# Optimization experiments

Measured on AMD Instinct MI355X. Metric: run time of the kernel, lower is better.

Reference implementation:

```python
import jax, jax.numpy as jnp
import numpy as np
import math
from functools import lru_cache

# ---- static configuration (matches init_kwargs) ----
B_IN = 24           # input bandwidth  -> spatial grid 2*B_IN = 48
B_OUT = 24          # output bandwidth (<= B_IN)
F_IN = 16           # nfeature_in
F_OUT = 16          # output_dim
BATCH = 16
N_ALPHA = 6
_alphas = np.arange(N_ALPHA) * (2.0 * np.pi / N_ALPHA)
_betas_g = np.array([np.pi / 16.0, np.pi / 8.0])
GRID = np.array([[a, b, 0.0] for a in _alphas for b in _betas_g])  # [12, 3] = (alpha, beta, gamma)
SCALING = 1.0 / math.sqrt(GRID.shape[0] * F_IN * (B_OUT ** 3) / (B_IN ** 3))

_LNF = np.array([math.lgamma(n + 1.0) for n in range(4 * max(B_IN, B_OUT) + 4)])  # log n!


def _wigner_d(l, beta):
    """Wigner small-d matrix d^l_{m'm}(beta); element [l+m', l+m]. numpy, float64."""
    m = np.arange(-l, l + 1)
    mp = m[:, None, None]          # m'
    mm = m[None, :, None]          # m
    k = np.arange(0, 2 * l + 1)[None, None, :]
    valid = (k >= np.maximum(0, mm - mp)) & (k <= np.minimum(l + mm, l - mp))
    kk = np.where(valid, k, 0)
    ln = (0.5 * (_LNF[l + mp] + _LNF[l - mp] + _LNF[l + mm] + _LNF[l - mm])
          - _LNF[np.where(valid, l + mm - k, 0)] - _LNF[kk]
          - _LNF[np.where(valid, mp - mm + k, 0)] - _LNF[np.where(valid, l - mp - k, 0)])
    sign = np.where((mp - mm + k) % 2 == 0, 1.0, -1.0)
    coef = np.where(valid, sign * np.exp(ln), 0.0)
    c, s = np.cos(beta / 2.0), np.sin(beta / 2.0)
    e_c = np.where(valid, 2 * l - 2 * k + mm - mp, 0)
    e_s = np.where(valid, 2 * k + mp - mm, 0)
    return (coef * (c ** e_c) * (s ** e_s)).sum(-1)  # [2l+1, 2l+1]


def _quad_weights(b):
    """Driscoll-Healy quadrature weights over beta, scaled so that
    sum_j w_j d^l_{mn}(b_j) d^{l'}_{mn}(b_j) = delta_{ll'} / (2l+1)."""
    k = np.arange(b)
    j = np.arange(2 * b)
    s = np.sin(np.outer(2 * j + 1, 2 * k + 1) * np.pi / (4.0 * b))
    w = (2.0 / b) * np.sin(np.pi * (2 * j + 1) / (4.0 * b)) * (s / (2 * k + 1)).sum(1)
    return w / 2.0


@lru_cache(maxsize=None)
def _wigner_betas(b, nl, weighted):
    """Per-degree wigner-d stacks at SOFT beta grid: tuple of [2b, 2l+1, 2l+1]."""
    betas = (np.arange(2 * b) + 0.5) * np.pi / (2 * b)
    w = _quad_weights(b)
    out = []
    for l in range(nl):
        d = np.stack([_wigner_d(l, be) for be in betas])  # [2b, 2l+1, 2l+1]
        d = d * (w[:, None, None] if weighted else float(2 * l + 1))
        out.append(jnp.asarray(d.astype(np.float32)))
    return tuple(out)


@lru_cache(maxsize=None)
def _so3_rft_matrix(b):
    """conj(D^l_{mn}(g_p)) for each grid rotation; [P, nspec] complex64."""
    mats = []
    for l in range(b):
        m = np.arange(-l, l + 1)
        rows = []
        for (al, be, ga) in GRID:
            D = np.exp(-1j * m[:, None] * al) * _wigner_d(l, be) * np.exp(-1j * m[None, :] * ga)
            rows.append(np.conj(D).reshape(-1))
        mats.append(np.stack(rows))  # [P, (2l+1)^2]
    return jnp.asarray(np.concatenate(mats, axis=1).astype(np.complex64))


def so3_rfft(x, b_out):
    # x: [Z, 2b, 2b, 2b] real, axes = (beta, alpha, gamma) -> [nspec, Z] complex
    b_in = x.shape[1] // 2
    X = jnp.fft.fftn(x.astype(jnp.complex64), axes=(2, 3))  # [Z, beta, m, n]
    wig = _wigner_betas(b_in, b_out, True)
    outs = []
    for l in range(b_out):
        idx = np.arange(-l, l + 1) % (2 * b_in)             # static FFT freq indices
        xx = X[:, :, idx[:, None], idx[None, :]]            # [Z, 2b, 2l+1, 2l+1]
        Fl = jnp.einsum('jmn,zjmn->mnz', wig[l], xx)        # beta quadrature
        outs.append(Fl.reshape((2 * l + 1) ** 2, -1))
    return jnp.concatenate(outs, axis=0)


def so3_mm(Fx, Fy, b):
    # Fx [nspec, B, f_in], Fy [nspec, f_in, f_out] -> [nspec, B, f_out]; per-degree block matmul
    outs, begin = [], 0
    for l in range(b):
        L = 2 * l + 1
        xl = Fx[begin:begin + L * L].reshape(L, L, Fx.shape[1], Fx.shape[2])
        yl = Fy[begin:begin + L * L].reshape(L, L, Fy.shape[1], Fy.shape[2])
        zl = jnp.einsum('mkbf,knfg->mnbg', xl, yl)
        outs.append(zl.reshape(L * L, Fx.shape[1], Fy.shape[2]))
        begin += L * L
    return jnp.concatenate(outs, axis=0)


def so3_rifft(Fz, b):
    # Fz [nspec, Z] complex -> [Z, 2b, 2b, 2b] real
    Z = Fz.shape[1]
    wig = _wigner_betas(b, b, False)
    S = jnp.zeros((Z, 2 * b, 2 * b, 2 * b), jnp.complex64)
    begin = 0
    for l in range(b):
        L = 2 * l + 1
        Fl = Fz[begin:begin + L * L].reshape(L, L, Z)
        sl = jnp.einsum('jmn,mnz->zjmn', wig[l], Fl)
        idx = np.arange(-l, l + 1) % (2 * b)
        S = S.at[:, :, idx[:, None], idx[None, :]].add(sl)
        begin += L * L
    return jnp.fft.ifftn(S, axes=(2, 3)).real.astype(jnp.float32)


def _forward(x, kernel):
    B = x.shape[0]
    z = x.reshape(B * F_IN, 2 * B_IN, 2 * B_IN, 2 * B_IN)
    Fx = so3_rfft(z, B_OUT).reshape(-1, B, F_IN)                      # [nspec, B, f_in]
    Fy = jnp.einsum('fgp,ps->sfg', (kernel * SCALING).astype(jnp.complex64),
                    _so3_rft_matrix(B_OUT))                           # [nspec, f_in, f_out]
    Fz = so3_mm(Fx, Fy, B_OUT)                                        # [nspec, B, f_out]
    out = so3_rifft(Fz.reshape(-1, B * F_OUT), B_OUT)
    return out.reshape(B, F_OUT, 2 * B_OUT, 2 * B_OUT, 2 * B_OUT)


def setup_inputs() -> dict:
    key = jax.random.key(0)
    k1, k2 = jax.random.split(key)
    x = jax.random.normal(k1, (BATCH, F_IN, 2 * B_IN, 2 * B_IN, 2 * B_IN), jnp.float32)
    kernel = jax.random.normal(k2, (F_IN, F_OUT, GRID.shape[0]), jnp.float32) * 0.05
    return {"x": x, "kernel": kernel}


def reference(x, kernel):
    return _forward(x, kernel)
```

## Files before the change

### kernel.cpp

```cpp
#include <hip/hip_runtime.h>
#include <math.h>

#define NSPEC 18424

static constexpr int OFF[25] = {0,1,10,35,84,165,286,455,680,969,1330,1771,2300,2925,
                                3654,4495,5456,6545,7770,9139,10660,12341,14190,16215,18424};
static constexpr int BACC[25] = {0,1,2,6,10,19,28,44,60,85,110,146,182,231,280,344,
                                 408,489,570,670,770,891,1012,1156,1300};
static constexpr double PI_D = 3.14159265358979323846264338327950288;
static constexpr float SCALING_F = 0.07216878364870322f;

__device__ __forceinline__ void cfma(float2& acc, float2 a, float2 b){
    acc.x += a.x*b.x - a.y*b.y;
    acc.y += a.x*b.y + a.y*b.x;
}

__global__ __launch_bounds__(256) void k0_wigner(float* __restrict__ wig_w,
                                                 float* __restrict__ wig_u,
                                                 float2* __restrict__ conjD){
    const int l = blockIdx.x, bi = blockIdx.y, L = 2*l+1;
    __shared__ double lnf[104];
    const int t = threadIdx.x;
    for (int i = t; i < 104; i += 256){
        double s = 0.0;
        for (int k = 2; k <= i; ++k) s += log((double)k);
        lnf[i] = s;
    }
    __syncthreads();
    double beta, alpha = 0.0, wq = 0.0;
    const bool isq = (bi < 48);
    if (isq){
        beta = (bi + 0.5)*PI_D/48.0;
        double acc = 0.0;
        for (int k = 0; k < 24; ++k)
            acc += sin((double)(2*bi+1)*(double)(2*k+1)*PI_D/96.0)/(double)(2*k+1);
        wq = (2.0/24.0)*sin(PI_D*(double)(2*bi+1)/96.0)*acc*0.5;
    } else {
        int p = bi - 48;
        alpha = (double)(p >> 1)*(PI_D/3.0);
        beta  = (p & 1) ? PI_D/8.0 : PI_D/16.0;
    }
    const double ch = cos(0.5*beta), sh = sin(0.5*beta);
    const double lc = log(ch), ls = log(sh);
    for (int e = t; e < L*L; e += 256){
        const int r = e / L, c = e % L;
        const int mp = r - l, mm = c - l;
        const int k0 = max(0, mm - mp), k1 = min(l + mm, l - mp);
        const double pre = 0.5*(lnf[l+mp] + lnf[l-mp] + lnf[l+mm] + lnf[l-mm]);
        double d = 0.0;
        for (int k = k0; k <= k1; ++k){
            const int ec = 2*l - 2*k + mm - mp, es = 2*k + mp - mm;
            const double term = exp(pre - lnf[l+mm-k] - lnf[k] - lnf[mp-mm+k]
                                    - lnf[l-mp-k] + (double)ec*lc + (double)es*ls);
            d += ((mp - mm + k) & 1) ? -term : term;
        }
        if (isq){
            const int idx = 48*OFF[l] + (bi*L + r)*L + c;
            wig_w[idx] = (float)(wq*d);
            wig_u[idx] = (float)((double)(2*l+1)*d);
        } else {
            const int p = bi - 48;
            conjD[(size_t)p*NSPEC + OFF[l] + r*L + c] =
                make_float2((float)(cos((double)mp*alpha)*d),
                            (float)(sin((double)mp*alpha)*d));
        }
    }
}

__global__ __launch_bounds__(256) void k_twiddles(float2* __restrict__ tw1a,
                                                  float2* __restrict__ tw1b,
                                                  float2* __restrict__ twI1,
                                                  float2* __restrict__ twI2){
    const int t = threadIdx.x;
    for (int i = t; i < 24*48; i += 256){
        int m = i/48, a = i%48;
        double th = 2.0*PI_D*(double)(m*a)/48.0;
        tw1a[i] = make_float2((float)cos(th), (float)(-sin(th)));
        twI2[i] = make_float2((float)cos(th), (float)sin(th));
    }
    for (int i = t; i < 48*48; i += 256){
        int n = i/48, c = i%48;
        double th = 2.0*PI_D*(double)(n*c)/48.0;
        tw1b[i] = make_float2((float)cos(th), (float)(-sin(th)));
    }
    for (int i = t; i < 47*48; i += 256){
        int nn = i/48, c = i%48;
        double th = 2.0*PI_D*(double)((nn-23)*c)/48.0;
        twI1[i] = make_float2((float)cos(th), (float)sin(th));
    }
}

__global__ __launch_bounds__(192) void k1a(const float* __restrict__ x,
                                           const float2* __restrict__ tw1a,
                                           float2* __restrict__ A1){
    const int j = blockIdx.x, z = blockIdx.y;
    __shared__ float xs[48*49];
    __shared__ float2 tws[24*48];
    for (int e = threadIdx.x; e < 1152; e += 192) tws[e] = tw1a[e];
    const float* src = x + (size_t)(z*48 + j)*2304;
    for (int e = threadIdx.x; e < 2304; e += 192)
        xs[(e/48)*49 + (e%48)] = src[e];
    __syncthreads();
    const int c = threadIdx.x % 48, mq = threadIdx.x / 48;
    float ar[6], ai[6];
    #pragma unroll
    for (int i = 0; i < 6; ++i){ ar[i] = 0.f; ai[i] = 0.f; }
    for (int a = 0; a < 48; ++a){
        const float xv = xs[a*49 + c];
        #pragma unroll
        for (int i = 0; i < 6; ++i){
            const float2 tw = tws[(mq*6 + i)*48 + a];
            ar[i] += xv*tw.x; ai[i] += xv*tw.y;
        }
    }
    #pragma unroll
    for (int i = 0; i < 6; ++i){
        const int m = mq*6 + i;
        A1[((size_t)(j*24 + m)*256 + z)*48 + c] = make_float2(ar[i], ai[i]);
    }
}

__global__ __launch_bounds__(256) void k1b(const float2* __restrict__ A1,
                                           const float2* __restrict__ tw1b,
                                           float2* __restrict__ Xf){
    const int m = blockIdx.x, j = blockIdx.y, zt = blockIdx.z;
    __shared__ float2 as_[48*129];
    __shared__ float2 tws[48*48];
    for (int e = threadIdx.x; e < 2304; e += 256) tws[e] = tw1b[e];
    const float2* src = A1 + ((size_t)(j*24 + m)*256 + zt*128)*48;
    for (int e = threadIdx.x; e < 6144; e += 256)
        as_[(e%48)*129 + (e/48)] = src[e];
    __syncthreads();
    const int z = threadIdx.x & 127, nh = threadIdx.x >> 7;
    float2 acc[24];
    #pragma unroll
    for (int i = 0; i < 24; ++i) acc[i] = make_float2(0.f, 0.f);
    for (int cc = 0; cc < 48; ++cc){
        const float2 xv = as_[cc*129 + z];
        #pragma unroll
        for (int i = 0; i < 24; ++i)
            cfma(acc[i], xv, tws[(nh*24 + i)*48 + cc]);
    }
    #pragma unroll
    for (int i = 0; i < 24; ++i){
        const int n = nh*24 + i;
        Xf[((size_t)(j*24 + m)*48 + n)*256 + zt*128 + z] = acc[i];
    }
}

__global__ __launch_bounds__(256) void k2(const float2* __restrict__ Xf,
                                          const float* __restrict__ wigw,
                                          float2* __restrict__ Fx){
    const int mf = (int)blockIdx.x - 23, nf = (int)blockIdx.y - 23;
    const int z = threadIdx.x;
    const int am = mf < 0 ? -mf : mf;
    const int anf = nf < 0 ? -nf : nf;
    const int lmin = am > anf ? am : anf;
    const int nidx = ((mf < 0 ? -nf : nf) + 48) % 48;
    const float sgn = mf < 0 ? -1.f : 1.f;
    float ar[24], ai[24];
    int widx[24];
    #pragma unroll
    for (int l = 0; l < 24; ++l){
        ar[l] = 0.f; ai[l] = 0.f;
        widx[l] = 48*OFF[l] + (l+mf)*(2*l+1) + (l+nf);
    }
    for (int j = 0; j < 48; ++j){
        const float2 xv = Xf[((size_t)(j*24 + am)*48 + nidx)*256 + z];
        const float xi = sgn*xv.y;
        #pragma unroll
        for (int l = 0; l < 24; ++l){
            if (l >= lmin){
                const float w = wigw[widx[l]];
                ar[l] += w*xv.x; ai[l] += w*xi;
            }
            widx[l] += (2*l+1)*(2*l+1);
        }
    }
    #pragma unroll
    for (int l = 0; l < 24; ++l){
        if (l >= lmin){
            const int L = 2*l+1;
            Fx[((size_t)(OFF[l] + (l+mf)*L + (l+nf)))*256 + z] = make_float2(ar[l], ai[l]);
        }
    }
}

__global__ __launch_bounds__(256) void k3(const float* __restrict__ kern,
                                          const float2* __restrict__ conjD,
                                          float2* __restrict__ Fy){
    const int s = blockIdx.x, t = threadIdx.x;
    float kr[12];
    #pragma unroll
    for (int p = 0; p < 12; ++p) kr[p] = kern[t*12 + p];
    float accr = 0.f, acci = 0.f;
    #pragma unroll
    for (int p = 0; p < 12; ++p){
        const float2 D = conjD[(size_t)p*NSPEC + s];
        accr += kr[p]*D.x; acci += kr[p]*D.y;
    }
    Fy[(size_t)s*256 + t] = make_float2(SCALING_F*accr, SCALING_F*acci);
}

__global__ __launch_bounds__(256) void k4g(const float2* __restrict__ Fx,
                                           const float2* __restrict__ Fy,
                                           float2* __restrict__ Fz){
    const int bid = blockIdx.x;
    int l = 0;
    #pragma unroll
    for (int i = 1; i < 24; ++i) if (bid >= BACC[i]) l = i;
    const int L = 2*l+1, CT = l/2 + 1;
    const int tb = bid - BACC[l];
    const int bm = tb / CT, bn = tb % CT;
    const int t = threadIdx.x;
    const int lane = t & 63, seg = t >> 6;
    const int tr = t >> 4, tc = t & 15;
    __shared__ float2 As[16*64];
    __shared__ float2 Bs[16*64];
    float2 acc[4][4];
    #pragma unroll
    for (int i = 0; i < 4; ++i)
        #pragma unroll
        for (int jj = 0; jj < 4; ++jj) acc[i][jj] = make_float2(0.f, 0.f);

    const int mr = bm*4 + seg;
    const int nc = bn*4 + seg;
    const bool va = (mr < L), vb = (nc < L);
    const float2* aPtr = Fx + (size_t)(OFF[l] + (va ? mr : 0)*L)*256 + lane*4;
    const float2* bPtr = Fy + (size_t)(OFF[l] + (vb ? nc : 0))*256 + lane*4;
    const int bA  = lane >> 2;
    const int fA0 = (lane & 3)*4;
    const int fB  = lane >> 2;
    const int gB0 = (lane & 3)*4;

    for (int k = 0; k < L; ++k){
        float2 a0={0,0},a1={0,0},a2={0,0},a3={0,0};
        float2 b0={0,0},b1={0,0},b2={0,0},b3={0,0};
        if (va){ const float2* p = aPtr + (size_t)k*256; a0=p[0]; a1=p[1]; a2=p[2]; a3=p[3]; }
        if (vb){ const float2* p = bPtr + (size_t)k*L*256; b0=p[0]; b1=p[1]; b2=p[2]; b3=p[3]; }
        __syncthreads();
        As[(fA0+0)*64 + seg*16 + bA] = a0;
        As[(fA0+1)*64 + seg*16 + bA] = a1;
        As[(fA0+2)*64 + seg*16 + bA] = a2;
        As[(fA0+3)*64 + seg*16 + bA] = a3;
        Bs[fB*64 + seg*16 + gB0 + 0] = b0;
        Bs[fB*64 + seg*16 + gB0 + 1] = b1;
        Bs[fB*64 + seg*16 + gB0 + 2] = b2;
        Bs[fB*64 + seg*16 + gB0 + 3] = b3;
        __syncthreads();
        #pragma unroll
        for (int f = 0; f < 16; ++f){
            float2 av0 = As[f*64 + tr*4 + 0];
            float2 av1 = As[f*64 + tr*4 + 1];
            float2 av2 = As[f*64 + tr*4 + 2];
            float2 av3 = As[f*64 + tr*4 + 3];
            float2 bv0 = Bs[f*64 + tc*4 + 0];
            float2 bv1 = Bs[f*64 + tc*4 + 1];
            float2 bv2 = Bs[f*64 + tc*4 + 2];
            float2 bv3 = Bs[f*64 + tc*4 + 3];
            cfma(acc[0][0], av0, bv0); cfma(acc[0][1], av0, bv1);
            cfma(acc[0][2], av0, bv2); cfma(acc[0][3], av0, bv3);
            cfma(acc[1][0], av1, bv0); cfma(acc[1][1], av1, bv1);
            cfma(acc[1][2], av1, bv2); cfma(acc[1][3], av1, bv3);
            cfma(acc[2][0], av2, bv0); cfma(acc[2][1], av2, bv1);
            cfma(acc[2][2], av2, bv2); cfma(acc[2][3], av2, bv3);
            cfma(acc[3][0], av3, bv0); cfma(acc[3][1], av3, bv1);
            cfma(acc[3][2], av3, bv2); cfma(acc[3][3], av3, bv3);
        }
    }
    #pragma unroll
    for (int i = 0; i < 4; ++i){
        const int r = tr*4 + i;
        const int mro = bm*4 + (r >> 4), b = r & 15;
        if (mro < L){
            #pragma unroll
            for (int jj = 0; jj < 4; ++jj){
                const int c = tc*4 + jj;
                const int nco = bn*4 + (c >> 4), g = c & 15;
                if (nco < L)
                    Fz[((size_t)(OFF[l] + mro*L + nco))*256 + b*16 + g] = acc[i][jj];
            }
        }
    }
}

__global__ __launch_bounds__(256) void k5(const float2* __restrict__ Fz,
                                          const float* __restrict__ wigu,
                                          float2* __restrict__ S){
    const int mf = blockIdx.x;
    const int nf = (int)blockIdx.y - 23;
    const int z = threadIdx.x;
    const int anf = nf < 0 ? -nf : nf;
    const int lmin = mf > anf ? mf : anf;
    float2 fz[24];
    int widx[24];
    #pragma unroll
    for (int l = 0; l < 24; ++l){
        const int L = 2*l+1;
        fz[l] = (l >= lmin) ? Fz[((size_t)(OFF[l] + (l+mf)*L + (l+nf)))*256 + z]
                            : make_float2(0.f, 0.f);
        widx[l] = 48*OFF[l] + (l+mf)*L + (l+nf);
    }
    const int nn = nf + 23;
    for (int j = 0; j < 48; ++j){
        float sr = 0.f, si = 0.f;
        #pragma unroll
        for (int l = 0; l < 24; ++l){
            if (l >= lmin){
                const float w = wigu[widx[l]];
                sr += w*fz[l].x; si += w*fz[l].y;
            }
            widx[l] += (2*l+1)*(2*l+1);
        }
        S[((size_t)(mf*47 + nn)*48 + j)*256 + z] = make_float2(sr, si);
    }
}

__global__ __launch_bounds__(256) void i1(const float2* __restrict__ S,
                                          const float2* __restrict__ twI1,
                                          float2* __restrict__ U){
    const int m = blockIdx.x, j = blockIdx.y, zt = blockIdx.z;
    __shared__ float2 sbuf[128*49];
    __shared__ float2 tws[47*48];
    for (int e = threadIdx.x; e < 2256; e += 256) tws[e] = twI1[e];
    for (int e = threadIdx.x; e < 47*128; e += 256){
        const int nn = e >> 7, zl = e & 127;
        sbuf[nn*128 + zl] = S[((size_t)(m*47 + nn)*48 + j)*256 + zt*128 + zl];
    }
    __syncthreads();
    const int z = threadIdx.x & 127, ch = threadIdx.x >> 7;
    float2 acc[24];
    #pragma unroll
    for (int i = 0; i < 24; ++i) acc[i] = make_float2(0.f, 0.f);
    for (int nn = 0; nn < 47; ++nn){
        const float2 sv = sbuf[nn*128 + z];
        #pragma unroll
        for (int i = 0; i < 24; ++i)
            cfma(acc[i], sv, tws[nn*48 + ch*24 + i]);
    }
    __syncthreads();
    #pragma unroll
    for (int i = 0; i < 24; ++i)
        sbuf[z*49 + ch*24 + i] = acc[i];
    __syncthreads();
    float2* dst = U + (size_t)(j*256 + zt*128)*1152 + m*48;
    for (int e = threadIdx.x; e < 6144; e += 256){
        const int zz = e/48, c = e%48;
        dst[(size_t)zz*1152 + c] = sbuf[zz*49 + c];
    }
}

__global__ __launch_bounds__(256) void i2(const float2* __restrict__ U,
                                          const float2* __restrict__ twI2,
                                          float* __restrict__ out){
    const int z = blockIdx.x, j = blockIdx.y;
    __shared__ float2 uv[24*49];
    __shared__ float2 tws[24*48];
    for (int e = threadIdx.x; e < 1152; e += 256) tws[e] = twI2[e];
    const float2* src = U + (size_t)(j*256 + z)*1152;
    for (int e = threadIdx.x; e < 1152; e += 256)
        uv[(e/48)*49 + (e%48)] = src[e];
    __syncthreads();
    float* dst = out + (size_t)(z*48 + j)*2304;
    for (int o = threadIdx.x; o < 2304; o += 256){
        const int a = o / 48, c = o % 48;
        float acc = uv[c].x;
        #pragma unroll
        for (int m = 1; m < 24; ++m){
            const float2 tw = tws[m*48 + a];
            const float2 u  = uv[m*49 + c];
            acc += 2.0f*(tw.x*u.x - tw.y*u.y);
        }
        dst[o] = acc*(1.0f/2304.0f);
    }
}

extern "C" void kernel_launch(void* const* d_in, const int* in_sizes, int n_in,
                              void* d_out, int out_size, void* d_ws, size_t ws_size,
                              hipStream_t stream){
    (void)in_sizes; (void)n_in; (void)out_size;
    const float* x    = (const float*)d_in[0];
    const float* kern = (const float*)d_in[1];
    float* out = (float*)d_out;

    char* ws = (char*)d_ws;
    size_t o = 0;
    auto nb = [&](size_t bytes){ size_t r = o; o += (bytes + 255) & ~(size_t)255; return r; };
    float*  wig_w = (float*) (ws + nb(884352ull*4));
    float*  wig_u = (float*) (ws + nb(884352ull*4));
    float2* conjD = (float2*)(ws + nb(221088ull*8));
    float2* tw1a  = (float2*)(ws + nb(1152ull*8));
    float2* tw1b  = (float2*)(ws + nb(2304ull*8));
    float2* twI1  = (float2*)(ws + nb(2256ull*8));
    float2* twI2  = (float2*)(ws + nb(1152ull*8));
    float2* big0  = (float2*)(ws + nb(14155776ull*8));
    float2* big1  = (float2*)(ws + nb(14155776ull*8));
    float2* Fx    = (float2*)(ws + nb(4716544ull*8));
    float2* Fy    = (float2*)(ws + nb(4716544ull*8));
    float2* Fz    = (float2*)(ws + nb(4716544ull*8));
    if (o > ws_size) return;

    k0_wigner <<<dim3(24,60),  dim3(256), 0, stream>>>(wig_w, wig_u, conjD);
    k_twiddles<<<dim3(1),      dim3(256), 0, stream>>>(tw1a, tw1b, twI1, twI2);
    k1a       <<<dim3(48,256), dim3(192), 0, stream>>>(x, tw1a, big0);
    k1b       <<<dim3(24,48,2),dim3(256), 0, stream>>>(big0, tw1b, big1);
    k2        <<<dim3(47,47),  dim3(256), 0, stream>>>(big1, wig_w, Fx);
    k3        <<<dim3(NSPEC),  dim3(256), 0, stream>>>(kern, conjD, Fy);
    k4g       <<<dim3(1300),   dim3(256), 0, stream>>>(Fx, Fy, Fz);
    k5        <<<dim3(24,47),  dim3(256), 0, stream>>>(Fz, wig_u, big0);
    i1        <<<dim3(24,48,2),dim3(256), 0, stream>>>(big0, twI1, big1);
    i2        <<<dim3(256,48), dim3(256), 0, stream>>>(big1, twI2, out);
}
```

Before: 1.823 ms.

## Exploit conjugate symmetry in k2/k4g, recurrence Wigner-d, drop twiddle LDS copies

```diff
diff --git a/kernel.cpp b/kernel.cpp
--- a/kernel.cpp
+++ b/kernel.cpp
@@ -5,8 +5,8 @@
 
 static constexpr int OFF[25] = {0,1,10,35,84,165,286,455,680,969,1330,1771,2300,2925,
                                 3654,4495,5456,6545,7770,9139,10660,12341,14190,16215,18424};
-static constexpr int BACC[25] = {0,1,2,6,10,19,28,44,60,85,110,146,182,231,280,344,
-                                 408,489,570,670,770,891,1012,1156,1300};
+static constexpr int P24[25] = {0,72,144,210,276,326,376,421,466,498,530,558,586,604,622,
+                                637,652,660,668,674,680,682,684,685,686};
 static constexpr double PI_D = 3.14159265358979323846264338327950288;
 static constexpr float SCALING_F = 0.07216878364870322f;
 
@@ -15,17 +15,47 @@
     acc.y += a.x*b.y + a.y*b.x;
 }
 
-__global__ __launch_bounds__(256) void k0_wigner(float* __restrict__ wig_w,
+__global__ __launch_bounds__(256) void k_tables(float2* __restrict__ tw1a,
+                                                float2* __restrict__ tw1b,
+                                                float2* __restrict__ twI1,
+                                                float2* __restrict__ twI2,
+                                                double* __restrict__ lnfg){
+    const int t = threadIdx.x;
+    __shared__ double lt[104];
+    if (t < 104) lt[t] = (t >= 2) ? log((double)t) : 0.0;
+    __syncthreads();
+    if (t == 0){
+        double run = 0.0;
+        for (int i = 0; i < 104; ++i){ run += lt[i]; lnfg[i] = run; }
+    }
+    for (int i = t; i < 24*48; i += 256){
+        int m = i/48, a = i%48;
+        double th = 2.0*PI_D*(double)(m*a)/48.0;
+        tw1a[i] = make_float2((float)cos(th), (float)(-sin(th)));
+        twI2[i] = make_float2((float)cos(th), (float)sin(th));
+    }
+    for (int i = t; i < 48*48; i += 256){
+        int n = i/48, c = i%48;
+        double th = 2.0*PI_D*(double)(n*c)/48.0;
+        tw1b[i] = make_float2((float)cos(th), (float)(-sin(th)));
+    }
+    for (int i = t; i < 47*48; i += 256){
+        int nn = i/48, c = i%48;
+        double th = 2.0*PI_D*(double)((nn-23)*c)/48.0;
+        twI1[i] = make_float2((float)cos(th), (float)sin(th));
+    }
+}
+
+__global__ __launch_bounds__(256) void k0_wigner(const double* __restrict__ lnfg,
+                                                 float* __restrict__ wig_w,
                                                  float* __restrict__ wig_u,
                                                  float2* __restrict__ conjD){
     const int l = blockIdx.x, bi = blockIdx.y, L = 2*l+1;
     __shared__ double lnf[104];
+    __shared__ double rcpt[105];
     const int t = threadIdx.x;
-    for (int i = t; i < 104; i += 256){
-        double s = 0.0;
-        for (int k = 2; k <= i; ++k) s += log((double)k);
-        lnf[i] = s;
-    }
+    for (int i = t; i < 104; i += 256) lnf[i] = lnfg[i];
+    for (int i = t; i < 105; i += 256) rcpt[i] = (i > 0) ? 1.0/(double)i : 0.0;
     __syncthreads();
     double beta, alpha = 0.0, wq = 0.0;
     const bool isq = (bi < 48);
@@ -42,17 +72,27 @@
     }
     const double ch = cos(0.5*beta), sh = sin(0.5*beta);
     const double lc = log(ch), ls = log(sh);
+    const double t2 = (sh/ch)*(sh/ch);
     for (int e = t; e < L*L; e += 256){
         const int r = e / L, c = e % L;
         const int mp = r - l, mm = c - l;
         const int k0 = max(0, mm - mp), k1 = min(l + mm, l - mp);
-        const double pre = 0.5*(lnf[l+mp] + lnf[l-mp] + lnf[l+mm] + lnf[l-mm]);
         double d = 0.0;
-        for (int k = k0; k <= k1; ++k){
-            const int ec = 2*l - 2*k + mm - mp, es = 2*k + mp - mm;
-            const double term = exp(pre - lnf[l+mm-k] - lnf[k] - lnf[mp-mm+k]
-                                    - lnf[l-mp-k] + (double)ec*lc + (double)es*ls);
-            d += ((mp - mm + k) & 1) ? -term : term;
+        if (k1 >= k0){
+            const double pre = 0.5*(lnf[l+mp] + lnf[l-mp] + lnf[l+mm] + lnf[l-mm]);
+            const int ec = 2*l - 2*k0 + mm - mp, es = 2*k0 + mp - mm;
+            double term = exp(pre - lnf[l+mm-k0] - lnf[k0] - lnf[mp-mm+k0] - lnf[l-mp-k0]
+                              + (double)ec*lc + (double)es*ls);
+            double sgn = ((mp - mm + k0) & 1) ? -1.0 : 1.0;
+            double n1 = (double)(l + mm - k0);
+            double n2 = (double)(l - mp - k0);
+            d = sgn*term;
+            for (int k = k0; k < k1; ++k){
+                term *= n1 * n2 * rcpt[k+1] * rcpt[mp-mm+k+1] * t2;
+                n1 -= 1.0; n2 -= 1.0;
+                sgn = -sgn;
+                d += sgn*term;
+            }
         }
         if (isq){
             const int idx = 48*OFF[l] + (bi*L + r)*L + c;
@@ -64,29 +104,6 @@
                 make_float2((float)(cos((double)mp*alpha)*d),
                             (float)(sin((double)mp*alpha)*d));
         }
-    }
-}
-
-__global__ __launch_bounds__(256) void k_twiddles(float2* __restrict__ tw1a,
-                                                  float2* __restrict__ tw1b,
-                                                  float2* __restrict__ twI1,
-                                                  float2* __restrict__ twI2){
-    const int t = threadIdx.x;
-    for (int i = t; i < 24*48; i += 256){
-        int m = i/48, a = i%48;
-        double th = 2.0*PI_D*(double)(m*a)/48.0;
-        tw1a[i] = make_float2((float)cos(th), (float)(-sin(th)));
-        twI2[i] = make_float2((float)cos(th), (float)sin(th));
-    }
-    for (int i = t; i < 48*48; i += 256){
-        int n = i/48, c = i%48;
-        double th = 2.0*PI_D*(double)(n*c)/48.0;
-        tw1b[i] = make_float2((float)cos(th), (float)(-sin(th)));
-    }
-    for (int i = t; i < 47*48; i += 256){
-        int nn = i/48, c = i%48;
-        double th = 2.0*PI_D*(double)((nn-23)*c)/48.0;
-        twI1[i] = make_float2((float)cos(th), (float)sin(th));
     }
 }
 
@@ -125,8 +142,6 @@
                                            float2* __restrict__ Xf){
     const int m = blockIdx.x, j = blockIdx.y, zt = blockIdx.z;
     __shared__ float2 as_[48*129];
-    __shared__ float2 tws[48*48];
-    for (int e = threadIdx.x; e < 2304; e += 256) tws[e] = tw1b[e];
     const float2* src = A1 + ((size_t)(j*24 + m)*256 + zt*128)*48;
     for (int e = threadIdx.x; e < 6144; e += 256)
         as_[(e%48)*129 + (e/48)] = src[e];
@@ -139,7 +154,7 @@
         const float2 xv = as_[cc*129 + z];
         #pragma unroll
         for (int i = 0; i < 24; ++i)
-            cfma(acc[i], xv, tws[(nh*24 + i)*48 + cc]);
+            cfma(acc[i], xv, tw1b[(nh*24 + i)*48 + cc]);
     }
     #pragma unroll
     for (int i = 0; i < 24; ++i){
@@ -151,13 +166,12 @@
 __global__ __launch_bounds__(256) void k2(const float2* __restrict__ Xf,
                                           const float* __restrict__ wigw,
                                           float2* __restrict__ Fx){
-    const int mf = (int)blockIdx.x - 23, nf = (int)blockIdx.y - 23;
+    const int mf = blockIdx.x;
+    const int nf = (int)blockIdx.y - 23;
     const int z = threadIdx.x;
-    const int am = mf < 0 ? -mf : mf;
     const int anf = nf < 0 ? -nf : nf;
-    const int lmin = am > anf ? am : anf;
-    const int nidx = ((mf < 0 ? -nf : nf) + 48) % 48;
-    const float sgn = mf < 0 ? -1.f : 1.f;
+    const int lmin = mf > anf ? mf : anf;
+    const int nidx = (nf + 48) % 48;
     float ar[24], ai[24];
     int widx[24];
     #pragma unroll
@@ -166,13 +180,12 @@
         widx[l] = 48*OFF[l] + (l+mf)*(2*l+1) + (l+nf);
     }
     for (int j = 0; j < 48; ++j){
-        const float2 xv = Xf[((size_t)(j*24 + am)*48 + nidx)*256 + z];
-        const float xi = sgn*xv.y;
+        const float2 xv = Xf[((size_t)(j*24 + mf)*48 + nidx)*256 + z];
         #pragma unroll
         for (int l = 0; l < 24; ++l){
             if (l >= lmin){
                 const float w = wigw[widx[l]];
-                ar[l] += w*xv.x; ai[l] += w*xi;
+                ar[l] += w*xv.x; ai[l] += w*xv.y;
             }
             widx[l] += (2*l+1)*(2*l+1);
         }
@@ -206,58 +219,70 @@
                                            const float2* __restrict__ Fy,
                                            float2* __restrict__ Fz){
     const int bid = blockIdx.x;
-    int l = 0;
-    #pragma unroll
-    for (int i = 1; i < 24; ++i) if (bid >= BACC[i]) l = i;
+    int idx = 0;
+    #pragma unroll
+    for (int i = 1; i < 24; ++i) if (bid >= P24[i]) idx = i;
+    const int l = 23 - idx;
     const int L = 2*l+1, CT = l/2 + 1;
-    const int tb = bid - BACC[l];
+    const int tb = bid - P24[idx];
     const int bm = tb / CT, bn = tb % CT;
+
     const int t = threadIdx.x;
-    const int lane = t & 63, seg = t >> 6;
-    const int tr = t >> 4, tc = t & 15;
+    const int lane = t & 63, w = t >> 6;
+    const int tc = t & 15, tr = t >> 4;
+
     __shared__ float2 As[16*64];
     __shared__ float2 Bs[16*64];
+
     float2 acc[4][4];
     #pragma unroll
     for (int i = 0; i < 4; ++i)
         #pragma unroll
         for (int jj = 0; jj < 4; ++jj) acc[i][jj] = make_float2(0.f, 0.f);
 
-    const int mr = bm*4 + seg;
-    const int nc = bn*4 + seg;
-    const bool va = (mr < L), vb = (nc < L);
-    const float2* aPtr = Fx + (size_t)(OFF[l] + (va ? mr : 0)*L)*256 + lane*4;
-    const float2* bPtr = Fy + (size_t)(OFF[l] + (vb ? nc : 0))*256 + lane*4;
-    const int bA  = lane >> 2;
-    const int fA0 = (lane & 3)*4;
-    const int fB  = lane >> 2;
-    const int gB0 = (lane & 3)*4;
+    const int mrA = l + bm*4 + w;
+    const int ncB = bn*4 + w;
+    const bool aok = (bm*4 + w <= l);
+    const bool bok = (ncB < L);
+    const float2* aBase = Fx + (size_t)(OFF[l] + mrA*L)*256 + lane*4;
+    const float2* bBase = Fy + (size_t)(OFF[l] + ncB)*256 + lane*4;
+
+    const int fA = (lane & 3)*4;
+    const int rA = w*16 + (lane >> 2);
+    const int fB = lane >> 2;
+    const int cB = w*16 + (lane & 3)*4;
+
+    float2 ra0={0,0}, ra1={0,0}, ra2={0,0}, ra3={0,0};
+    float2 rb0={0,0}, rb1={0,0}, rb2={0,0}, rb3={0,0};
+    if (aok){ const float2* p = aBase; ra0=p[0]; ra1=p[1]; ra2=p[2]; ra3=p[3]; }
+    if (bok){ const float2* p = bBase; rb0=p[0]; rb1=p[1]; rb2=p[2]; rb3=p[3]; }
 
     for (int k = 0; k < L; ++k){
-        float2 a0={0,0},a1={0,0},a2={0,0},a3={0,0};
-        float2 b0={0,0},b1={0,0},b2={0,0},b3={0,0};
-        if (va){ const float2* p = aPtr + (size_t)k*256; a0=p[0]; a1=p[1]; a2=p[2]; a3=p[3]; }
-        if (vb){ const float2* p = bPtr + (size_t)k*L*256; b0=p[0]; b1=p[1]; b2=p[2]; b3=p[3]; }
         __syncthreads();
-        As[(fA0+0)*64 + seg*16 + bA] = a0;
-        As[(fA0+1)*64 + seg*16 + bA] = a1;
-        As[(fA0+2)*64 + seg*16 + bA] = a2;
-        As[(fA0+3)*64 + seg*16 + bA] = a3;
-        Bs[fB*64 + seg*16 + gB0 + 0] = b0;
-        Bs[fB*64 + seg*16 + gB0 + 1] = b1;
-        Bs[fB*64 + seg*16 + gB0 + 2] = b2;
-        Bs[fB*64 + seg*16 + gB0 + 3] = b3;
+        As[(fA+0)*64 + rA] = ra0;
+        As[(fA+1)*64 + rA] = ra1;
+        As[(fA+2)*64 + rA] = ra2;
+        As[(fA+3)*64 + rA] = ra3;
+        {
+            float4* bp = (float4*)&Bs[fB*64 + cB];
+            bp[0] = make_float4(rb0.x, rb0.y, rb1.x, rb1.y);
+            bp[1] = make_float4(rb2.x, rb2.y, rb3.x, rb3.y);
+        }
         __syncthreads();
+        if (k + 1 < L){
+            if (aok){ const float2* p = aBase + (size_t)(k+1)*256; ra0=p[0]; ra1=p[1]; ra2=p[2]; ra3=p[3]; }
+            if (bok){ const float2* p = bBase + (size_t)(k+1)*L*256; rb0=p[0]; rb1=p[1]; rb2=p[2]; rb3=p[3]; }
+        }
         #pragma unroll
         for (int f = 0; f < 16; ++f){
-            float2 av0 = As[f*64 + tr*4 + 0];
-            float2 av1 = As[f*64 + tr*4 + 1];
-            float2 av2 = As[f*64 + tr*4 + 2];
-            float2 av3 = As[f*64 + tr*4 + 3];
-            float2 bv0 = Bs[f*64 + tc*4 + 0];
-            float2 bv1 = Bs[f*64 + tc*4 + 1];
-            float2 bv2 = Bs[f*64 + tc*4 + 2];
-            float2 bv3 = Bs[f*64 + tc*4 + 3];
+            const float2 av0 = As[f*64 + tr];
+            const float2 av1 = As[f*64 + tr + 16];
+            const float2 av2 = As[f*64 + tr + 32];
+            const float2 av3 = As[f*64 + tr + 48];
+            const float2 bv0 = Bs[f*64 + tc];
+            const float2 bv1 = Bs[f*64 + tc + 16];
+            const float2 bv2 = Bs[f*64 + tc + 32];
+            const float2 bv3 = Bs[f*64 + tc + 48];
             cfma(acc[0][0], av0, bv0); cfma(acc[0][1], av0, bv1);
             cfma(acc[0][2], av0, bv2); cfma(acc[0][3], av0, bv3);
             cfma(acc[1][0], av1, bv0); cfma(acc[1][1], av1, bv1);
@@ -270,15 +295,13 @@
     }
     #pragma unroll
     for (int i = 0; i < 4; ++i){
-        const int r = tr*4 + i;
-        const int mro = bm*4 + (r >> 4), b = r & 15;
-        if (mro < L){
+        if (bm*4 + i <= l){
+            const int mro = l + bm*4 + i;
             #pragma unroll
             for (int jj = 0; jj < 4; ++jj){
-                const int c = tc*4 + jj;
-                const int nco = bn*4 + (c >> 4), g = c & 15;
+                const int nco = bn*4 + jj;
                 if (nco < L)
-                    Fz[((size_t)(OFF[l] + mro*L + nco))*256 + b*16 + g] = acc[i][jj];
+                    Fz[((size_t)(OFF[l] + mro*L + nco))*256 + t] = acc[i][jj];
             }
         }
     }
@@ -321,8 +344,6 @@
                                           float2* __restrict__ U){
     const int m = blockIdx.x, j = blockIdx.y, zt = blockIdx.z;
     __shared__ float2 sbuf[128*49];
-    __shared__ float2 tws[47*48];
-    for (int e = threadIdx.x; e < 2256; e += 256) tws[e] = twI1[e];
     for (int e = threadIdx.x; e < 47*128; e += 256){
         const int nn = e >> 7, zl = e & 127;
         sbuf[nn*128 + zl] = S[((size_t)(m*47 + nn)*48 + j)*256 + zt*128 + zl];
@@ -336,7 +357,7 @@
         const float2 sv = sbuf[nn*128 + z];
         #pragma unroll
         for (int i = 0; i < 24; ++i)
-            cfma(acc[i], sv, tws[nn*48 + ch*24 + i]);
+            cfma(acc[i], sv, twI1[nn*48 + ch*24 + i]);
     }
     __syncthreads();
     #pragma unroll
@@ -393,6 +414,7 @@
     float2* tw1b  = (float2*)(ws + nb(2304ull*8));
     float2* twI1  = (float2*)(ws + nb(2256ull*8));
     float2* twI2  = (float2*)(ws + nb(1152ull*8));
+    double* lnfg  = (double*)(ws + nb(104ull*8));
     float2* big0  = (float2*)(ws + nb(14155776ull*8));
     float2* big1  = (float2*)(ws + nb(14155776ull*8));
     float2* Fx    = (float2*)(ws + nb(4716544ull*8));
@@ -400,13 +422,13 @@
     float2* Fz    = (float2*)(ws + nb(4716544ull*8));
     if (o > ws_size) return;
 
-    k0_wigner <<<dim3(24,60),  dim3(256), 0, stream>>>(wig_w, wig_u, conjD);
-    k_twiddles<<<dim3(1),      dim3(256), 0, stream>>>(tw1a, tw1b, twI1, twI2);
+    k_tables  <<<dim3(1),      dim3(256), 0, stream>>>(tw1a, tw1b, twI1, twI2, lnfg);
+    k0_wigner <<<dim3(24,60),  dim3(256), 0, stream>>>(lnfg, wig_w, wig_u, conjD);
     k1a       <<<dim3(48,256), dim3(192), 0, stream>>>(x, tw1a, big0);
     k1b       <<<dim3(24,48,2),dim3(256), 0, stream>>>(big0, tw1b, big1);
-    k2        <<<dim3(47,47),  dim3(256), 0, stream>>>(big1, wig_w, Fx);
+    k2        <<<dim3(24,47),  dim3(256), 0, stream>>>(big1, wig_w, Fx);
     k3        <<<dim3(NSPEC),  dim3(256), 0, stream>>>(kern, conjD, Fy);
-    k4g       <<<dim3(1300),   dim3(256), 0, stream>>>(Fx, Fy, Fz);
+    k4g       <<<dim3(686),    dim3(256), 0, stream>>>(Fx, Fy, Fz);
     k5        <<<dim3(24,47),  dim3(256), 0, stream>>>(Fz, wig_u, big0);
     i1        <<<dim3(24,48,2),dim3(256), 0, stream>>>(big0, twI1, big1);
     i2        <<<dim3(256,48), dim3(256), 0, stream>>>(big1, twI2, out);
```

Result: faster. 1.586 ms (-13.0%).
